# Kernel tuning notes

Hardware: AMD Instinct MI355X
Metric: run time of the kernel (lower is better)

## Reference

```python
import jax, jax.numpy as jnp
import numpy as np

B, T, D, H, L, OUT = 512, 82, 129, 1024, 2, 128
TOTAL_LEN = 182  # decoder runs TOTAL_LEN - T = 100 steps


def setup_inputs() -> dict:
    key = jax.random.key(0)
    ks = jax.random.split(key, 32)
    s = 1.0 / np.sqrt(H)  # torch LSTM default init scale
    def p(k, shape):
        return jax.random.uniform(k, shape, dtype=jnp.float32, minval=-s, maxval=s)
    inp = {}
    inp["x"] = jax.random.normal(ks[0], (B, T, D), dtype=jnp.float32)
    inp["lengths"] = jax.random.randint(ks[1], (B,), 1, T + 1, dtype=jnp.int32)
    idx = 2
    for pre, in0 in (("enc", D), ("dec", D - 1)):
        dims = [in0, H]
        for l in range(L):
            inp[f"{pre}_Wih{l}"] = p(ks[idx], (4 * H, dims[l])); idx += 1
            inp[f"{pre}_Whh{l}"] = p(ks[idx], (4 * H, H)); idx += 1
            inp[f"{pre}_bih{l}"] = p(ks[idx], (4 * H,)); idx += 1
            inp[f"{pre}_bhh{l}"] = p(ks[idx], (4 * H,)); idx += 1
    inp["fc_W"] = p(ks[idx], (OUT, H)); idx += 1
    inp["fc_b"] = p(ks[idx], (OUT,))
    return inp


def _cell(x, h, c, Wih, Whh, bih, bhh):
    # torch gate order: i, f, g, o
    g = x @ Wih.T + h @ Whh.T + (bih + bhh)
    i, f, gg, o = jnp.split(g, 4, axis=-1)
    c_new = jax.nn.sigmoid(f) * c + jax.nn.sigmoid(i) * jnp.tanh(gg)
    h_new = jax.nn.sigmoid(o) * jnp.tanh(c_new)
    return h_new, c_new


def _forward(x, lengths, enc, dec, fc_W, fc_b):
    Bsz, Tlen, _ = x.shape
    h0 = jnp.zeros((L, Bsz, H), x.dtype)
    c0 = jnp.zeros((L, Bsz, H), x.dtype)
    xs = jnp.swapaxes(x, 0, 1)  # [T, B, D]
    # packed-sequence semantics: state frozen once t >= lengths[b]
    mask = (jnp.arange(Tlen)[:, None] < lengths[None, :])[..., None]  # [T, B, 1]

    def enc_step(carry, inp):
        h, c = carry
        xt, m = inp
        layer_in = xt
        hs, cs = [], []
        for l in range(L):
            hn, cn = _cell(layer_in, h[l], c[l], *enc[l])
            hn = jnp.where(m, hn, h[l])
            cn = jnp.where(m, cn, c[l])
            hs.append(hn); cs.append(cn)
            layer_in = hn
        return (jnp.stack(hs), jnp.stack(cs)), None

    (h, c), _ = jax.lax.scan(enc_step, (h0, c0), (xs, mask))

    steps = TOTAL_LEN - Tlen
    x0 = jnp.zeros((Bsz, D - 1), x.dtype)

    def dec_step(carry, _):
        h, c, xt = carry
        layer_in = xt
        hs, cs = [], []
        for l in range(L):
            hn, cn = _cell(layer_in, h[l], c[l], *dec[l])
            hs.append(hn); cs.append(cn)
            layer_in = hn
        out = layer_in @ fc_W.T + fc_b  # [B, OUT]
        return (jnp.stack(hs), jnp.stack(cs), out), out

    _, outs = jax.lax.scan(dec_step, (h, c, x0), None, length=steps)
    return jnp.swapaxes(outs, 0, 1)  # [B, steps, OUT]


def reference(x, lengths,
              enc_Wih0, enc_Whh0, enc_bih0, enc_bhh0,
              enc_Wih1, enc_Whh1, enc_bih1, enc_bhh1,
              dec_Wih0, dec_Whh0, dec_bih0, dec_bhh0,
              dec_Wih1, dec_Whh1, dec_bih1, dec_bhh1,
              fc_W, fc_b):
    enc = [(enc_Wih0, enc_Whh0, enc_bih0, enc_bhh0),
           (enc_Wih1, enc_Whh1, enc_bih1, enc_bhh1)]
    dec = [(dec_Wih0, dec_Whh0, dec_bih0, dec_bhh0),
           (dec_Wih1, dec_Whh1, dec_bih1, dec_bhh1)]
    return _forward(x, lengths, enc, dec, fc_W, fc_b)
```

## Files before the change

kernel.cpp:

```cpp
#include <hip/hip_runtime.h>
#include <stdint.h>

#define BB 512
#define TT 82
#define DD 129
#define DXP 192
#define HH 1024
#define G4 4096
#define NOUT 128
#define NSTEPS 100

typedef unsigned short u16;
typedef __attribute__((ext_vector_type(8))) _Float16 f16x8;
typedef __attribute__((ext_vector_type(8))) short short8;
typedef __attribute__((ext_vector_type(4))) float f32x4;

__device__ __forceinline__ u16 f2h(float f) {
  _Float16 h = (_Float16)f;
  return __builtin_bit_cast(u16, h);
}
__device__ __forceinline__ float sigm(float x) { return 1.f / (1.f + __expf(-x)); }
__device__ __forceinline__ float tanhfast(float x) {
  float ax = fabsf(x);
  float e = __expf(2.f * ax);
  float t = 1.f - 2.f / (e + 1.f);
  return copysignf(t, x);
}
__device__ __forceinline__ void glds16(const void* g, void* l) {
  __builtin_amdgcn_global_load_lds((const __attribute__((address_space(1))) void*)g,
                                   (__attribute__((address_space(3))) void*)l, 16, 0, 0);
}

struct GemmP {
  const u16* A0; const u16* W0; const u16* A1; const u16* W1;
  const float* bias; float* cst; u16* hnext;
  int K0, K1, t;
};

template <int FUSE>
__global__ __launch_bounds__(256) void step_gemm(
    GemmP q0, GemmP q1, const int* __restrict__ lengths, float* __restrict__ fout)
{
  const GemmP p = (blockIdx.z == 0) ? q0 : q1;
  __shared__ __align__(16) u16 At[2][64 * 64];
  __shared__ __align__(16) u16 Bt[2][64 * 64];
  const int tid = threadIdx.x;
  const int lane = tid & 63;
  const int w = tid >> 6;
  const int m0 = blockIdx.y * 64;
  const int n0 = blockIdx.x * 64;

  const int nIter0 = p.K0 >> 6;
  const int nIterT = nIter0 + (p.K1 >> 6);

  auto stage = [&](int i, int buf) {
    const u16* A; const u16* W; int K; int kb;
    if (i < nIter0) { A = p.A0; W = p.W0; K = p.K0; kb = i << 6; }
    else            { A = p.A1; W = p.W1; K = p.K1; kb = (i - nIter0) << 6; }
    #pragma unroll
    for (int j = 0; j < 2; ++j) {
      int slot = tid + j * 256;
      int r = slot >> 3, c = slot & 7;
      int g = c ^ (r & 7);
      glds16(A + (size_t)(m0 + r) * K + kb + g * 8,
             &At[buf][(j * 256 + w * 64) * 8]);
    }
    #pragma unroll
    for (int j = 0; j < 2; ++j) {
      int slot = tid + j * 256;
      int r = slot >> 3, c = slot & 7;
      int g = c ^ (r & 7);
      glds16(W + (size_t)(n0 + r) * K + kb + g * 8,
             &Bt[buf][(j * 256 + w * 64) * 8]);
    }
  };

  f32x4 acc[4] = {};

  stage(0, 0);
  for (int i = 0; i < nIterT; ++i) {
    __syncthreads();
    if (i + 1 < nIterT) stage(i + 1, (i + 1) & 1);
    const int buf = i & 1;
    #pragma unroll
    for (int kc = 0; kc < 2; ++kc) {
      f16x8 af, bfr[4];
      const int gch = kc * 4 + (lane >> 4);
      {
        int r = w * 16 + (lane & 15);
        int c = gch ^ (r & 7);
        af = __builtin_bit_cast(f16x8, *(const short8*)&At[buf][(r * 8 + c) * 8]);
      }
      #pragma unroll
      for (int tj = 0; tj < 4; ++tj) {
        int r = tj * 16 + (lane & 15);
        int c = gch ^ (r & 7);
        bfr[tj] = __builtin_bit_cast(f16x8, *(const short8*)&Bt[buf][(r * 8 + c) * 8]);
      }
      #pragma unroll
      for (int tj = 0; tj < 4; ++tj)
        acc[tj] = __builtin_amdgcn_mfma_f32_16x16x32_f16(af, bfr[tj], acc[tj], 0, 0, 0);
    }
  }
  __syncthreads();

  const int col = lane & 15;
  const int rq = (lane >> 4) << 2;

  if (FUSE == 1) {
    const int j = blockIdx.x * 16 + col;
    float bv[4];
    #pragma unroll
    for (int tj = 0; tj < 4; ++tj) bv[tj] = p.bias[n0 + tj * 16 + col];
    const int mb = m0 + w * 16 + rq;
    #pragma unroll
    for (int r = 0; r < 4; ++r) {
      const int m = mb + r;
      const size_t idx = ((size_t)m << 10) + j;
      const bool upd = (p.t < 0) || (p.t < lengths[m]);
      if (upd) {
        float cv = p.cst[idx];
        float gi = acc[0][r] + bv[0];
        float gf = acc[1][r] + bv[1];
        float gg = acc[2][r] + bv[2];
        float go = acc[3][r] + bv[3];
        float cn = sigm(gf) * cv + sigm(gi) * tanhfast(gg);
        float hn = sigm(go) * tanhfast(cn);
        p.cst[idx] = cn;
        p.hnext[idx] = f2h(hn);
      } else {
        p.hnext[idx] = p.A0[idx];
      }
    }
  } else {
    const int mb = m0 + w * 16 + rq;
    #pragma unroll
    for (int tj = 0; tj < 4; ++tj) {
      const int n = n0 + tj * 16 + col;
      const float bv = p.bias[n];
      #pragma unroll
      for (int r = 0; r < 4; ++r) {
        const int m = mb + r;
        const float v = acc[tj][r] + bv;
        if (FUSE == 0) {
          fout[(size_t)m * (NSTEPS * NOUT) + n] = v;
        } else {
          fout[((size_t)(m & (BB - 1)) * NSTEPS + (m >> 9)) * NOUT + n] = v;
        }
      }
    }
  }
}

__global__ void conv_wp(const float* __restrict__ w, u16* __restrict__ wb,
                        int C, int Cp, int R, int perm, int total)
{
  int idx = blockIdx.x * 256 + threadIdx.x;
  if (idx >= total) return;
  int cc = idx % Cp;
  int n = idx / Cp;
  int orig = perm ? (((n >> 4) & 3) * (R >> 2) + (n >> 6) * 16 + (n & 15)) : n;
  wb[idx] = f2h(cc < C ? w[(size_t)orig * C + cc] : 0.f);
}

__global__ void conv_b(const float* __restrict__ b1, const float* __restrict__ b2,
                       float* __restrict__ bp)
{
  int n = blockIdx.x * 256 + threadIdx.x;
  if (n >= G4) return;
  int orig = ((n >> 4) & 3) * HH + (n >> 6) * 16 + (n & 15);
  bp[n] = b1[orig] + b2[orig];
}

__global__ void weff_kernel(const float* __restrict__ wih0, const float* __restrict__ fcW,
                            u16* __restrict__ weffb)
{
  int idx = blockIdx.x * 256 + threadIdx.x;
  int k = idx & (HH - 1);
  int n = idx >> 10;
  int orig = ((n >> 4) & 3) * HH + (n >> 6) * 16 + (n & 15);
  float s = 0.f;
  #pragma unroll 4
  for (int j = 0; j < NOUT; ++j) s += wih0[orig * NOUT + j] * fcW[(size_t)j * HH + k];
  weffb[idx] = f2h(s);
}

__global__ void beff_kernel(const float* __restrict__ bih, const float* __restrict__ bhh,
                            const float* __restrict__ wih0, const float* __restrict__ fcb,
                            float* __restrict__ bp)
{
  int n = blockIdx.x * 256 + threadIdx.x;
  if (n >= G4) return;
  int orig = ((n >> 4) & 3) * HH + (n >> 6) * 16 + (n & 15);
  float s = bih[orig] + bhh[orig];
  #pragma unroll 4
  for (int j = 0; j < NOUT; ++j) s += wih0[orig * NOUT + j] * fcb[j];
  bp[n] = s;
}

__global__ void conv_x(const float* __restrict__ x, u16* __restrict__ xb)
{
  int idx = blockIdx.x * 256 + threadIdx.x;
  if (idx >= TT * BB * DXP) return;
  int k = idx % DXP;
  int tb = idx / DXP;
  int b = tb & (BB - 1);
  int t = tb / BB;
  xb[idx] = f2h(k < DD ? x[((size_t)b * TT + t) * DD + k] : 0.f);
}

extern "C" void kernel_launch(void* const* d_in, const int* in_sizes, int n_in,
                              void* d_out, int out_size, void* d_ws, size_t ws_size,
                              hipStream_t stream) {
  (void)in_sizes; (void)n_in; (void)out_size;
  const float* x     = (const float*)d_in[0];
  const int*   lens  = (const int*)d_in[1];
  const float* eWih0 = (const float*)d_in[2];
  const float* eWhh0 = (const float*)d_in[3];
  const float* ebih0 = (const float*)d_in[4];
  const float* ebhh0 = (const float*)d_in[5];
  const float* eWih1 = (const float*)d_in[6];
  const float* eWhh1 = (const float*)d_in[7];
  const float* ebih1 = (const float*)d_in[8];
  const float* ebhh1 = (const float*)d_in[9];
  const float* dWih0 = (const float*)d_in[10];
  const float* dWhh0 = (const float*)d_in[11];
  const float* dbih0 = (const float*)d_in[12];
  const float* dbhh0 = (const float*)d_in[13];
  const float* dWih1 = (const float*)d_in[14];
  const float* dWhh1 = (const float*)d_in[15];
  const float* dbih1 = (const float*)d_in[16];
  const float* dbhh1 = (const float*)d_in[17];
  const float* fcW   = (const float*)d_in[18];
  const float* fcb   = (const float*)d_in[19];
  float* out = (float*)d_out;

  char* p = (char*)d_ws;
  auto carve = [&](size_t bytes) -> void* {
    void* q = (void*)p;
    p += (bytes + 255) & ~(size_t)255;
    return q;
  };
  u16* eWih0b = (u16*)carve((size_t)G4 * DXP * 2);
  u16* eWhh0b = (u16*)carve((size_t)G4 * HH * 2);
  u16* eWih1b = (u16*)carve((size_t)G4 * HH * 2);
  u16* eWhh1b = (u16*)carve((size_t)G4 * HH * 2);
  u16* Weffb  = (u16*)carve((size_t)G4 * HH * 2);
  u16* dWhh0b = (u16*)carve((size_t)G4 * HH * 2);
  u16* dWih1b = (u16*)carve((size_t)G4 * HH * 2);
  u16* dWhh1b = (u16*)carve((size_t)G4 * HH * 2);
  u16* fcWb   = (u16*)carve((size_t)NOUT * HH * 2);
  float* be0  = (float*)carve((size_t)G4 * 4);
  float* be1  = (float*)carve((size_t)G4 * 4);
  float* beff0= (float*)carve((size_t)G4 * 4);
  float* bd1  = (float*)carve((size_t)G4 * 4);
  u16* xb     = (u16*)carve((size_t)TT * BB * DXP * 2);
  u16* h0p[2] = { (u16*)carve((size_t)BB * HH * 2), (u16*)carve((size_t)BB * HH * 2) };
  u16* h1p[2] = { (u16*)carve((size_t)BB * HH * 2), (u16*)carve((size_t)BB * HH * 2) };
  float* c0   = (float*)carve((size_t)BB * HH * 4);
  float* c1   = (float*)carve((size_t)BB * HH * 4);
  u16* h1hist = (u16*)carve((size_t)(NSTEPS + 1) * BB * HH * 2);
  const size_t need = (size_t)(p - (char*)d_ws);
  const bool bigws = ws_size >= need;

  auto cw = [&](const float* src, u16* dst, int C, int Cp, int R, int perm) {
    int total = R * Cp;
    conv_wp<<<dim3((total + 255) / 256), dim3(256), 0, stream>>>(src, dst, C, Cp, R, perm, total);
  };
  cw(eWih0, eWih0b, DD, DXP, G4, 1);
  cw(eWhh0, eWhh0b, HH, HH, G4, 1);
  cw(eWih1, eWih1b, HH, HH, G4, 1);
  cw(eWhh1, eWhh1b, HH, HH, G4, 1);
  cw(dWhh0, dWhh0b, HH, HH, G4, 1);
  cw(dWih1, dWih1b, HH, HH, G4, 1);
  cw(dWhh1, dWhh1b, HH, HH, G4, 1);
  cw(fcW, fcWb, HH, HH, NOUT, 0);
  weff_kernel<<<dim3(G4 * HH / 256), dim3(256), 0, stream>>>(dWih0, fcW, Weffb);
  conv_b<<<dim3(16), dim3(256), 0, stream>>>(ebih0, ebhh0, be0);
  conv_b<<<dim3(16), dim3(256), 0, stream>>>(ebih1, ebhh1, be1);
  beff_kernel<<<dim3(16), dim3(256), 0, stream>>>(dbih0, dbhh0, dWih0, fcb, beff0);
  conv_b<<<dim3(16), dim3(256), 0, stream>>>(dbih1, dbhh1, bd1);
  conv_x<<<dim3((TT * BB * DXP + 255) / 256), dim3(256), 0, stream>>>(x, xb);

  hipMemsetAsync(h0p[0], 0, (size_t)BB * HH * 2, stream);
  hipMemsetAsync(h1p[0], 0, (size_t)BB * HH * 2, stream);
  hipMemsetAsync(c0, 0, (size_t)BB * HH * 4, stream);
  hipMemsetAsync(c1, 0, (size_t)BB * HH * 4, stream);

  const dim3 g1(64, 8, 1);
  const dim3 g2(64, 8, 2);

  auto L0 = [&](int t) -> GemmP {
    return GemmP{ h0p[t & 1], eWhh0b, xb + (size_t)t * BB * DXP, eWih0b,
                  be0, c0, h0p[(t + 1) & 1], HH, DXP, t };
  };
  auto L1e = [&](int t, u16* dst) -> GemmP {
    return GemmP{ h1p[t & 1], eWhh1b, h0p[(t + 1) & 1], eWih1b,
                  be1, c1, dst, HH, HH, t };
  };

  step_gemm<1><<<g1, 256, 0, stream>>>(L0(0), L0(0), lens, nullptr);
  for (int t = 0; t < TT - 1; ++t)
    step_gemm<1><<<g2, 256, 0, stream>>>(L1e(t, h1p[(t + 1) & 1]), L0(t + 1), lens, nullptr);
  u16* h1final = bigws ? h1hist : h1p[TT & 1];
  step_gemm<1><<<g1, 256, 0, stream>>>(L1e(TT - 1, h1final), L1e(TT - 1, h1final), lens, nullptr);

  if (bigws) {
    auto hs = [&](int s) { return h1hist + (size_t)s * BB * HH; };
    for (int s = 0; s < NSTEPS; ++s) {
      GemmP dl0{ h0p[s & 1], dWhh0b, hs(s), Weffb,
                 beff0, c0, h0p[(s + 1) & 1], HH, HH, -1 };
      step_gemm<1><<<g1, 256, 0, stream>>>(dl0, dl0, lens, nullptr);
      GemmP dl1{ hs(s), dWhh1b, h0p[(s + 1) & 1], dWih1b,
                 bd1, c1, hs(s + 1), HH, HH, -1 };
      step_gemm<1><<<g1, 256, 0, stream>>>(dl1, dl1, lens, nullptr);
    }
    GemmP pfc{ hs(1), fcWb, nullptr, nullptr, fcb, nullptr, nullptr, HH, 0, -1 };
    step_gemm<2><<<dim3(2, (NSTEPS * BB) / 64, 1), 256, 0, stream>>>(pfc, pfc, nullptr, out);
  } else {
    for (int s = 0; s < NSTEPS; ++s) {
      GemmP dl0{ h0p[s & 1], dWhh0b, h1p[s & 1], Weffb,
                 beff0, c0, h0p[(s + 1) & 1], HH, HH, -1 };
      step_gemm<1><<<g1, 256, 0, stream>>>(dl0, dl0, lens, nullptr);
      GemmP dl1{ h1p[s & 1], dWhh1b, h0p[(s + 1) & 1], dWih1b,
                 bd1, c1, h1p[(s + 1) & 1], HH, HH, -1 };
      step_gemm<1><<<g1, 256, 0, stream>>>(dl1, dl1, lens, nullptr);
      GemmP pfc{ h1p[(s + 1) & 1], fcWb, nullptr, nullptr, fcb, nullptr, nullptr, HH, 0, -1 };
      step_gemm<0><<<dim3(2, 8, 1), 256, 0, stream>>>(pfc, pfc, nullptr, out + (size_t)s * NOUT);
    }
  }
}
```

Measured before the change: 7.853 ms.

## Split decoder LSTM GEMMs into precomputed recurrent halves paired across layers

Each decoder layer's gate GEMM is split into a recurrent half, computed one launch early into an fp32 scratch buffer, and an input half that adds the scratch and applies the cell update. Independent halves from the two layers are batched into one two-slice launch. This doubles the blocks per launch and halves the K per block, aiming for better occupancy and a shorter per-step critical path. It adds 8 MB of scratch writes and reads per partial GEMM.

```diff
diff --git a/kernel.cpp b/kernel.cpp
--- a/kernel.cpp
+++ b/kernel.cpp
@@ -35,6 +35,7 @@
   const u16* A0; const u16* W0; const u16* A1; const u16* W1;
   const float* bias; float* cst; u16* hnext;
   int K0, K1, t;
+  float* scratch; int mode;
 };
 
 template <int FUSE>
@@ -108,28 +109,42 @@
   const int rq = (lane >> 4) << 2;
 
   if (FUSE == 1) {
-    const int j = blockIdx.x * 16 + col;
-    float bv[4];
-    #pragma unroll
-    for (int tj = 0; tj < 4; ++tj) bv[tj] = p.bias[n0 + tj * 16 + col];
     const int mb = m0 + w * 16 + rq;
-    #pragma unroll
-    for (int r = 0; r < 4; ++r) {
-      const int m = mb + r;
-      const size_t idx = ((size_t)m << 10) + j;
-      const bool upd = (p.t < 0) || (p.t < lengths[m]);
-      if (upd) {
-        float cv = p.cst[idx];
-        float gi = acc[0][r] + bv[0];
-        float gf = acc[1][r] + bv[1];
-        float gg = acc[2][r] + bv[2];
-        float go = acc[3][r] + bv[3];
-        float cn = sigm(gf) * cv + sigm(gi) * tanhfast(gg);
-        float hn = sigm(go) * tanhfast(cn);
-        p.cst[idx] = cn;
-        p.hnext[idx] = f2h(hn);
-      } else {
-        p.hnext[idx] = p.A0[idx];
+    if (p.mode == 2) {
+      #pragma unroll
+      for (int tj = 0; tj < 4; ++tj) {
+        const int n = n0 + tj * 16 + col;
+        #pragma unroll
+        for (int r = 0; r < 4; ++r)
+          p.scratch[((size_t)(mb + r) << 12) + n] = acc[tj][r];
+      }
+    } else {
+      const int j = blockIdx.x * 16 + col;
+      float bv[4];
+      #pragma unroll
+      for (int tj = 0; tj < 4; ++tj) bv[tj] = p.bias[n0 + tj * 16 + col];
+      #pragma unroll
+      for (int r = 0; r < 4; ++r) {
+        const int m = mb + r;
+        const size_t idx = ((size_t)m << 10) + j;
+        const bool upd = (p.t < 0) || (p.t < lengths[m]);
+        if (upd) {
+          float g[4];
+          #pragma unroll
+          for (int tj = 0; tj < 4; ++tj) g[tj] = acc[tj][r] + bv[tj];
+          if (p.mode == 1) {
+            #pragma unroll
+            for (int tj = 0; tj < 4; ++tj)
+              g[tj] += p.scratch[((size_t)m << 12) + n0 + tj * 16 + col];
+          }
+          float cv = p.cst[idx];
+          float cn = sigm(g[1]) * cv + sigm(g[0]) * tanhfast(g[2]);
+          float hn = sigm(g[3]) * tanhfast(cn);
+          p.cst[idx] = cn;
+          p.hnext[idx] = f2h(hn);
+        } else {
+          p.hnext[idx] = p.A0[idx];
+        }
       }
     }
   } else {
@@ -259,6 +274,8 @@
   u16* h1p[2] = { (u16*)carve((size_t)BB * HH * 2), (u16*)carve((size_t)BB * HH * 2) };
   float* c0   = (float*)carve((size_t)BB * HH * 4);
   float* c1   = (float*)carve((size_t)BB * HH * 4);
+  float* scr0 = (float*)carve((size_t)BB * G4 * 4);
+  float* scr1 = (float*)carve((size_t)BB * G4 * 4);
   u16* h1hist = (u16*)carve((size_t)(NSTEPS + 1) * BB * HH * 2);
   const size_t need = (size_t)(p - (char*)d_ws);
   const bool bigws = ws_size >= need;
@@ -292,40 +309,55 @@
 
   auto L0 = [&](int t) -> GemmP {
     return GemmP{ h0p[t & 1], eWhh0b, xb + (size_t)t * BB * DXP, eWih0b,
-                  be0, c0, h0p[(t + 1) & 1], HH, DXP, t };
+                  be0, c0, h0p[(t + 1) & 1], HH, DXP, t, nullptr, 0 };
   };
   auto L1e = [&](int t, u16* dst) -> GemmP {
     return GemmP{ h1p[t & 1], eWhh1b, h0p[(t + 1) & 1], eWih1b,
-                  be1, c1, dst, HH, HH, t };
+                  be1, c1, dst, HH, HH, t, nullptr, 0 };
   };
 
   step_gemm<1><<<g1, 256, 0, stream>>>(L0(0), L0(0), lens, nullptr);
   for (int t = 0; t < TT - 1; ++t)
     step_gemm<1><<<g2, 256, 0, stream>>>(L1e(t, h1p[(t + 1) & 1]), L0(t + 1), lens, nullptr);
-  u16* h1final = bigws ? h1hist : h1p[TT & 1];
-  step_gemm<1><<<g1, 256, 0, stream>>>(L1e(TT - 1, h1final), L1e(TT - 1, h1final), lens, nullptr);
 
   if (bigws) {
     auto hs = [&](int s) { return h1hist + (size_t)s * BB * HH; };
+    GemmP pa00{ h0p[0], dWhh0b, nullptr, nullptr, nullptr, nullptr, nullptr,
+                HH, 0, -1, scr0, 2 };
+    step_gemm<1><<<g2, 256, 0, stream>>>(L1e(TT - 1, hs(0)), pa00, lens, nullptr);
+
     for (int s = 0; s < NSTEPS; ++s) {
-      GemmP dl0{ h0p[s & 1], dWhh0b, hs(s), Weffb,
-                 beff0, c0, h0p[(s + 1) & 1], HH, HH, -1 };
-      step_gemm<1><<<g1, 256, 0, stream>>>(dl0, dl0, lens, nullptr);
-      GemmP dl1{ hs(s), dWhh1b, h0p[(s + 1) & 1], dWih1b,
-                 bd1, c1, hs(s + 1), HH, HH, -1 };
-      step_gemm<1><<<g1, 256, 0, stream>>>(dl1, dl1, lens, nullptr);
-    }
-    GemmP pfc{ hs(1), fcWb, nullptr, nullptr, fcb, nullptr, nullptr, HH, 0, -1 };
+      GemmP d0b{ hs(s), Weffb, nullptr, nullptr, beff0, c0, h0p[(s + 1) & 1],
+                 HH, 0, -1, scr0, 1 };
+      GemmP d1a{ hs(s), dWhh1b, nullptr, nullptr, nullptr, nullptr, nullptr,
+                 HH, 0, -1, scr1, 2 };
+      step_gemm<1><<<g2, 256, 0, stream>>>(d0b, d1a, lens, nullptr);
+
+      GemmP d1b{ h0p[(s + 1) & 1], dWih1b, nullptr, nullptr, bd1, c1, hs(s + 1),
+                 HH, 0, -1, scr1, 1 };
+      if (s + 1 < NSTEPS) {
+        GemmP d0a{ h0p[(s + 1) & 1], dWhh0b, nullptr, nullptr, nullptr, nullptr, nullptr,
+                   HH, 0, -1, scr0, 2 };
+        step_gemm<1><<<g2, 256, 0, stream>>>(d1b, d0a, lens, nullptr);
+      } else {
+        step_gemm<1><<<g1, 256, 0, stream>>>(d1b, d1b, lens, nullptr);
+      }
+    }
+    GemmP pfc{ hs(1), fcWb, nullptr, nullptr, fcb, nullptr, nullptr, HH, 0, -1,
+               nullptr, 0 };
     step_gemm<2><<<dim3(2, (NSTEPS * BB) / 64, 1), 256, 0, stream>>>(pfc, pfc, nullptr, out);
   } else {
+    step_gemm<1><<<g1, 256, 0, stream>>>(L1e(TT - 1, h1p[TT & 1]),
+                                         L1e(TT - 1, h1p[TT & 1]), lens, nullptr);
     for (int s = 0; s < NSTEPS; ++s) {
       GemmP dl0{ h0p[s & 1], dWhh0b, h1p[s & 1], Weffb,
-                 beff0, c0, h0p[(s + 1) & 1], HH, HH, -1 };
+                 beff0, c0, h0p[(s + 1) & 1], HH, HH, -1, nullptr, 0 };
       step_gemm<1><<<g1, 256, 0, stream>>>(dl0, dl0, lens, nullptr);
       GemmP dl1{ h1p[s & 1], dWhh1b, h0p[(s + 1) & 1], dWih1b,
-                 bd1, c1, h1p[(s + 1) & 1], HH, HH, -1 };
+                 bd1, c1, h1p[(s + 1) & 1], HH, HH, -1, nullptr, 0 };
       step_gemm<1><<<g1, 256, 0, stream>>>(dl1, dl1, lens, nullptr);
-      GemmP pfc{ h1p[(s + 1) & 1], fcWb, nullptr, nullptr, fcb, nullptr, nullptr, HH, 0, -1 };
+      GemmP pfc{ h1p[(s + 1) & 1], fcWb, nullptr, nullptr, fcb, nullptr, nullptr,
+                 HH, 0, -1, nullptr, 0 };
       step_gemm<0><<<dim3(2, 8, 1), 256, 0, stream>>>(pfc, pfc, nullptr, out + (size_t)s * NOUT);
     }
   }
```

Result: faster. 6.441 ms (-18.0%).
